# Performance work log

Measured on AMD Instinct MI355X. Metric: run time of the kernel, lower is better.

The kernel has to match this reference:

```python
import jax, jax.numpy as jnp
import numpy as np

S, LC = 8192, 16
CE = CH = 64      # char embed == char hidden (original quirk)
WE, HW = 128, 256 # word embed, word hidden
WV, CV, TAGS = 50000, 128, 50


def _lstm_step(h, c, x, Wih, Whh, bih, bhh):
    # PyTorch LSTM gate order: i, f, g, o
    g = x @ Wih.T + h @ Whh.T + bih + bhh
    i, f, gg, o = jnp.split(g, 4, axis=-1)
    c = jax.nn.sigmoid(f) * c + jax.nn.sigmoid(i) * jnp.tanh(gg)
    h = jax.nn.sigmoid(o) * jnp.tanh(c)
    return h, c


def setup_inputs() -> dict:
    key = jax.random.key(0)
    ks = jax.random.split(key, 16)
    inp = {
        'word_idxs': jax.random.randint(ks[0], (S,), 0, WV),
        'char_idxs': jax.random.randint(ks[1], (S, LC), 0, CV),
        'char_lens': jax.random.randint(ks[2], (S,), 1, LC + 1),
        'char_emb': jax.random.normal(ks[3], (CV, CE), jnp.float32) * 0.1,
        'char_Wih': jax.random.normal(ks[4], (4 * CH, CE), jnp.float32) * 0.1,
        'char_Whh': jax.random.normal(ks[5], (4 * CH, CH), jnp.float32) * 0.1,
        'char_bih': jax.random.normal(ks[6], (4 * CH,), jnp.float32) * 0.1,
        'char_bhh': jax.random.normal(ks[7], (4 * CH,), jnp.float32) * 0.1,
        'word_emb': jax.random.normal(ks[8], (WV, WE), jnp.float32) * 0.1,
        'word_Wih': jax.random.normal(ks[9], (4 * HW, WE + CH), jnp.float32) * 0.1,
        'word_Whh': jax.random.normal(ks[10], (4 * HW, HW), jnp.float32) * 0.1,
        'word_bih': jax.random.normal(ks[11], (4 * HW,), jnp.float32) * 0.1,
        'word_bhh': jax.random.normal(ks[12], (4 * HW,), jnp.float32) * 0.1,
        'tag_W': jax.random.normal(ks[13], (TAGS, HW), jnp.float32) * 0.1,
        'tag_b': jax.random.normal(ks[14], (TAGS,), jnp.float32) * 0.1,
    }
    return inp


def reference(word_idxs, char_idxs, char_lens,
              char_emb, char_Wih, char_Whh, char_bih, char_bhh,
              word_emb, word_Wih, word_Whh, word_bih, word_bhh,
              tag_W, tag_b):
    # --- char LSTM over all words in parallel (one fused scan over char time) ---
    cx = char_emb[char_idxs]                      # [S, LC, CE]
    cx = jnp.transpose(cx, (1, 0, 2))             # [LC, S, CE]

    def cstep(carry, x_t):
        h, c = carry
        h, c = _lstm_step(h, c, x_t, char_Wih, char_Whh, char_bih, char_bhh)
        return (h, c), h

    h0 = jnp.zeros((S, CH), cx.dtype)
    (_, _), hs = jax.lax.scan(cstep, (h0, h0), cx)  # hs: [LC, S, CH]
    # original takes char_lstm_out[-1] == hidden at position len(chars)-1
    char_feat = hs[char_lens - 1, jnp.arange(S)]    # [S, CH]

    # --- word LSTM over the sentence (batch = 1) ---
    wx = jnp.concatenate([word_emb[word_idxs], char_feat], axis=-1)  # [S, WE+CH]

    def wstep(carry, x_t):
        h, c = carry
        h, c = _lstm_step(h, c, x_t, word_Wih, word_Whh, word_bih, word_bhh)
        return (h, c), h

    wh0 = jnp.zeros((HW,), wx.dtype)
    (_, _), outs = jax.lax.scan(wstep, (wh0, wh0), wx)  # [S, HW]

    logits = outs @ tag_W.T + tag_b                     # [S, TAGS]
    return jax.nn.log_softmax(logits, axis=-1)
```

## Files before the change

kernel.cpp:

```cpp
#include <hip/hip_runtime.h>
#include <hip/hip_bf16.h>

#define S_LEN 8192
#define LC 16
#define CE 64
#define CH 64
#define WE 128
#define NTAGS 50

using bf16 = __hip_bfloat16;
typedef unsigned int u32;
typedef unsigned long long u64;

__device__ __forceinline__ float bfbits2f(unsigned short u) {
    union { unsigned int i; float f; } v; v.i = ((unsigned int)u) << 16; return v.f;
}
__device__ __forceinline__ float sigm(float x) {
    return __builtin_amdgcn_rcpf(1.0f + __expf(-x));
}
__device__ __forceinline__ float tanh_fast(float x) {
    return 1.0f - 2.0f * __builtin_amdgcn_rcpf(__expf(2.0f * x) + 1.0f);
}

template <bool BF>
__device__ __forceinline__ float ld1(const void* p, size_t i) {
    if constexpr (BF) return bfbits2f(((const unsigned short*)p)[i]);
    else              return ((const float*)p)[i];
}
template <bool BF>
__device__ __forceinline__ float4 ld4(const void* p, size_t i) {
    if constexpr (BF) {
        const ushort4 s = *reinterpret_cast<const ushort4*>((const unsigned short*)p + i);
        return make_float4(bfbits2f(s.x), bfbits2f(s.y), bfbits2f(s.z), bfbits2f(s.w));
    } else {
        return *reinterpret_cast<const float4*>((const float*)p + i);
    }
}
template <bool BF>
__device__ __forceinline__ void st1(void* p, size_t i, float v) {
    if constexpr (BF) ((bf16*)p)[i] = __float2bfloat16(v);
    else              ((float*)p)[i] = v;
}

__global__ void kdetect(const void* emb, u32* flag) {
    const int j = threadIdx.x;
    int s = 0;
    #pragma unroll
    for (int k = 0; k < 4; ++k) {
        const unsigned short u = ((const unsigned short*)emb)[j * 4 + k];
        const int e = (u >> 7) & 0xFF;
        s += (e >= 100 && e <= 133) ? 1 : 0;
    }
    #pragma unroll
    for (int off = 32; off >= 1; off >>= 1) s += __shfl_xor(s, off, 64);
    if (j == 0) *flag = (s >= 200) ? 1u : 0u;
}

template <bool BF>
__global__ __launch_bounds__(256, 2) void kchar(
        const u32* __restrict__ dtf,
        const int* __restrict__ char_idxs, const int* __restrict__ char_lens,
        const void* __restrict__ char_emb,
        const void* __restrict__ Wih, const void* __restrict__ Whh,
        const void* __restrict__ bih, const void* __restrict__ bhh,
        float* __restrict__ cfeat) {
    if ((*dtf != 0u) != BF) return;
    const int j = threadIdx.x;
    const int w0 = blockIdx.x * 8;

    __shared__ __align__(16) float emb_lds[128 * CE];
    __shared__ __align__(16) float gates_lds[8 * 256];
    __shared__ __align__(16) float h_lds[8 * CH];
    __shared__ __align__(16) float c_lds[8 * CH];
    __shared__ int cidx_lds[8 * LC];
    __shared__ int len_lds[8];

    {
        float4* emb4 = reinterpret_cast<float4*>(emb_lds);
        #pragma unroll
        for (int i = 0; i < 8; ++i) {
            const int c = i * 256 + j;
            emb4[c] = ld4<BF>(char_emb, (size_t)c * 4);
        }
    }
    if (j < 128) cidx_lds[j] = char_idxs[w0 * LC + j];
    if (j < 8)   len_lds[j]  = char_lens[w0 + j];
    h_lds[j] = 0.f; h_lds[j + 256] = 0.f;
    c_lds[j] = 0.f; c_lds[j + 256] = 0.f;

    float4 wih4[16], whh4[16];
    #pragma unroll
    for (int kc = 0; kc < 16; ++kc) {
        wih4[kc] = ld4<BF>(Wih, (size_t)j * CE + kc * 4);
        whh4[kc] = ld4<BF>(Whh, (size_t)j * CH + kc * 4);
    }
    const float bias = ld1<BF>(bih, j) + ld1<BF>(bhh, j);
    __syncthreads();

    for (int t = 0; t < LC; ++t) {
        for (int w = 0; w < 8; ++w) {
            const int ci = cidx_lds[w * LC + t];
            const float4* x4  = reinterpret_cast<const float4*>(emb_lds + ci * CE);
            const float4* hh4 = reinterpret_cast<const float4*>(h_lds + w * CH);
            float a0 = 0.f, a1 = 0.f, a2 = 0.f, a3 = 0.f;
            #pragma unroll
            for (int kc = 0; kc < 16; ++kc) {
                const float4 xv = x4[kc]; const float4 hv = hh4[kc];
                const float4 wi = wih4[kc]; const float4 wh = whh4[kc];
                a0 = fmaf(wi.x, xv.x, a0); a1 = fmaf(wi.y, xv.y, a1);
                a2 = fmaf(wi.z, xv.z, a2); a3 = fmaf(wi.w, xv.w, a3);
                a0 = fmaf(wh.x, hv.x, a0); a1 = fmaf(wh.y, hv.y, a1);
                a2 = fmaf(wh.z, hv.z, a2); a3 = fmaf(wh.w, hv.w, a3);
            }
            gates_lds[w * 256 + j] = bias + ((a0 + a1) + (a2 + a3));
        }
        __syncthreads();
        #pragma unroll
        for (int rep = 0; rep < 2; ++rep) {
            const int p = j + rep * 256;
            const int w = p >> 6, u = p & 63;
            const float ig = gates_lds[w * 256 + u];
            const float fg = gates_lds[w * 256 + 64 + u];
            const float gg = gates_lds[w * 256 + 128 + u];
            const float og = gates_lds[w * 256 + 192 + u];
            const float cn = sigm(fg) * c_lds[p] + sigm(ig) * tanh_fast(gg);
            const float hn = sigm(og) * tanh_fast(cn);
            c_lds[p] = cn; h_lds[p] = hn;
            if (t == len_lds[w] - 1)
                cfeat[(size_t)(w0 + w) * CH + u] = hn;
        }
        __syncthreads();
    }
}

template <bool BF>
__global__ __launch_bounds__(256) void kgx(
        const u32* __restrict__ dtf,
        int t0, const int* __restrict__ word_idxs, const float* __restrict__ cfeat,
        const void* __restrict__ wemb, const void* __restrict__ Wih,
        const void* __restrict__ bih, const void* __restrict__ bhh,
        float* __restrict__ Gxr) {
    if ((*dtf != 0u) != BF) return;
    const int j = threadIdx.x;
    const int wr0 = blockIdx.x * 16;
    const int w0g = t0 + wr0;
    __shared__ __align__(16) float wx[16 * 192];
    __shared__ int widx[16];
    if (j < 16) widx[j] = word_idxs[w0g + j];
    __syncthreads();
    {
        const int w = j >> 4, ch = j & 15;
        const size_t eb = (size_t)widx[w] * WE + ch * 8;
        const float4 f0 = ld4<BF>(wemb, eb), f1 = ld4<BF>(wemb, eb + 4);
        float4* dst = reinterpret_cast<float4*>(wx + w * 192 + ch * 8);
        dst[0] = f0; dst[1] = f1;
        const float4 cf = *reinterpret_cast<const float4*>(
            cfeat + (size_t)(w0g + w) * CH + ch * 4);
        *reinterpret_cast<float4*>(wx + w * 192 + WE + ch * 4) = cf;
    }
    __syncthreads();

    for (int g = 0; g < 4; ++g) {
        const int r = g * 256 + j;
        float acc[16];
        #pragma unroll
        for (int w = 0; w < 16; ++w) acc[w] = 0.f;
        #pragma unroll 8
        for (int kc = 0; kc < 48; ++kc) {
            const float4 wv = ld4<BF>(Wih, (size_t)r * 192 + kc * 4);
            #pragma unroll
            for (int w = 0; w < 16; ++w) {
                const float4 xv = *reinterpret_cast<const float4*>(wx + w * 192 + kc * 4);
                acc[w] = fmaf(wv.x, xv.x, acc[w]);
                acc[w] = fmaf(wv.y, xv.y, acc[w]);
                acc[w] = fmaf(wv.z, xv.z, acc[w]);
                acc[w] = fmaf(wv.w, xv.w, acc[w]);
            }
        }
        const float bias = ld1<BF>(bih, r) + ld1<BF>(bhh, r);
        #pragma unroll
        for (int w = 0; w < 16; ++w)
            Gxr[(size_t)(wr0 + w) * 1024 + r] = acc[w] + bias;
    }
}

template <bool BF>
__global__ __launch_bounds__(512, 1) void kwlstm(
        const u32* __restrict__ dtf,
        int t0, int t1, const void* __restrict__ whh, const float* __restrict__ Gxr,
        float* __restrict__ hallr, u64* hgx2, float* csave, u32* xccpub) {
    if ((*dtf != 0u) != BF) return;
    const int j = threadIdx.x;

    __shared__ int role_s;
    if (j == 0) {
        const u32 xcc = __builtin_amdgcn_s_getreg(6164) & 0xFu;
        __hip_atomic_store(&xccpub[blockIdx.x], 0xE0000000u | xcc,
                           __ATOMIC_RELAXED, __HIP_MEMORY_SCOPE_AGENT);
    }
    if (j < 64) {
        u32 v;
        do {
            v = __hip_atomic_load(&xccpub[j], __ATOMIC_RELAXED,
                                  __HIP_MEMORY_SCOPE_AGENT);
        } while ((v >> 24) != 0xE0u);
        const u32 v0 = __shfl(v, 0, 64);
        const u64 mask = __ballot((v & 0xFu) == (v0 & 0xFu));
        const int myb = blockIdx.x;
        int role = -1;
        if (__popcll(mask) >= 4) {
            if ((mask >> myb) & 1ull) {
                const int rank = __popcll(mask & ((1ull << myb) - 1ull));
                if (rank < 4) role = rank;
            }
        } else {
            if (myb < 4) role = myb;
        }
        if (j == 0) role_s = role;
    }
    __syncthreads();
    const int b = role_s;
    if (b < 0) return;

    const int r  = j & 255;
    const int kh = j >> 8;
    const int R  = ((r >> 6) << 8) + b * 64 + (r & 63);

    __shared__ __align__(16) float h_cur[256];
    __shared__ __align__(16) float part[512];
    __shared__ __align__(16) float gates[256];

    float4 wv[32];
    #pragma unroll
    for (int kc = 0; kc < 32; ++kc)
        wv[kc] = ld4<BF>(whh, (size_t)R * 256 + kh * 128 + kc * 4);

    if (j < 256) h_cur[j] = 0.f;
    float c_reg = 0.f;
    if (t0 > 0 && j < 64) c_reg = csave[b * 64 + j];

    float gx_cur = (j < 256) ? Gxr[(size_t)0 * 1024 + R] : 0.f;
    __syncthreads();

    for (int t = t0; t < t1; ++t) {
        if (t > 0 && j < 256) {
            u64 pk;
            do {
                pk = __hip_atomic_load(&hgx2[(size_t)(t & 1) * 256 + j],
                                       __ATOMIC_RELAXED, __HIP_MEMORY_SCOPE_AGENT);
            } while ((u32)(pk >> 32) != (u32)t);
            h_cur[j] = __uint_as_float((u32)pk);
        }
        __syncthreads();
        float gx_next = 0.f;
        if (t + 1 < t1 && j < 256)
            gx_next = Gxr[(size_t)(t + 1 - t0) * 1024 + R];
        float a0 = 0.f, a1 = 0.f, a2 = 0.f, a3 = 0.f;
        const float4* h4 = reinterpret_cast<const float4*>(h_cur) + kh * 32;
        #pragma unroll
        for (int kc = 0; kc < 32; ++kc) {
            const float4 hv = h4[kc];
            a0 = fmaf(wv[kc].x, hv.x, a0);
            a1 = fmaf(wv[kc].y, hv.y, a1);
            a2 = fmaf(wv[kc].z, hv.z, a2);
            a3 = fmaf(wv[kc].w, hv.w, a3);
        }
        part[j] = (a0 + a1) + (a2 + a3);
        __syncthreads();
        if (j < 256) gates[j] = part[j] + part[j + 256] + gx_cur;
        __syncthreads();
        if (j < 64) {
            const float ig = gates[j], fg = gates[64 + j];
            const float gg = gates[128 + j], og = gates[192 + j];
            const float cn = sigm(fg) * c_reg + sigm(ig) * tanh_fast(gg);
            c_reg = cn;
            const float hn = sigm(og) * tanh_fast(cn);
            hallr[(size_t)(t - t0) * 256 + b * 64 + j] = hn;
            const u64 pk = ((u64)(u32)(t + 1) << 32) | (u64)__float_as_uint(hn);
            __hip_atomic_store(&hgx2[(size_t)((t + 1) & 1) * 256 + b * 64 + j], pk,
                               __ATOMIC_RELAXED, __HIP_MEMORY_SCOPE_AGENT);
        }
        gx_cur = gx_next;
    }
    if (j < 64) csave[b * 64 + j] = c_reg;
}

template <bool BF>
__global__ __launch_bounds__(64) void ktag(
        const u32* __restrict__ dtf,
        int t0, const float* __restrict__ hallr, const void* __restrict__ tagW,
        const void* __restrict__ tagb, void* __restrict__ out) {
    if ((*dtf != 0u) != BF) return;
    const int tr = blockIdx.x, j = threadIdx.x;
    const int t = t0 + tr;
    __shared__ __align__(16) float4 h4[64];
    h4[j] = reinterpret_cast<const float4*>(hallr + (size_t)tr * 256)[j];
    __syncthreads();
    float logit = -1e30f;
    if (j < NTAGS) {
        float a0 = 0.f, a1 = 0.f, a2 = 0.f, a3 = 0.f;
        #pragma unroll
        for (int kc = 0; kc < 64; ++kc) {
            const float4 wvv = ld4<BF>(tagW, (size_t)j * 256 + kc * 4);
            const float4 hv = h4[kc];
            a0 = fmaf(wvv.x, hv.x, a0); a1 = fmaf(wvv.y, hv.y, a1);
            a2 = fmaf(wvv.z, hv.z, a2); a3 = fmaf(wvv.w, hv.w, a3);
        }
        logit = ld1<BF>(tagb, j) + ((a0 + a1) + (a2 + a3));
    }
    float m = logit;
    #pragma unroll
    for (int off = 32; off >= 1; off >>= 1) m = fmaxf(m, __shfl_xor(m, off, 64));
    const float e = (j < NTAGS) ? __expf(logit - m) : 0.f;
    float ssum = e;
    #pragma unroll
    for (int off = 32; off >= 1; off >>= 1) ssum += __shfl_xor(ssum, off, 64);
    if (j < NTAGS)
        st1<BF>(out, (size_t)t * NTAGS + j, logit - m - __logf(ssum));
}

extern "C" void kernel_launch(void* const* d_in, const int* in_sizes, int n_in,
                              void* d_out, int out_size, void* d_ws, size_t ws_size,
                              hipStream_t stream) {
    const int*  word_idxs = (const int*)d_in[0];
    const int*  char_idxs = (const int*)d_in[1];
    const int*  char_lens = (const int*)d_in[2];
    const void* char_emb  = d_in[3];
    const void* char_Wih  = d_in[4];
    const void* char_Whh  = d_in[5];
    const void* char_bih  = d_in[6];
    const void* char_bhh  = d_in[7];
    const void* word_emb  = d_in[8];
    const void* word_Wih  = d_in[9];
    const void* word_Whh  = d_in[10];
    const void* word_bih  = d_in[11];
    const void* word_bhh  = d_in[12];
    const void* tag_W     = d_in[13];
    const void* tag_b     = d_in[14];

    char* ws = (char*)d_ws;
    u32*   dtf    = (u32*)(ws);
    u64*   hgx2   = (u64*)(ws + 64);
    float* csave  = (float*)(ws + 4224);
    u32*   xccpub = (u32*)(ws + 5248);
    float* cfeat  = (float*)(ws + 8192);
    const size_t ring0 = 8192 + (size_t)S_LEN * CH * 4;

    int NC = 256;
    const int ncs[9] = {1, 2, 4, 8, 16, 32, 64, 128, 256};
    for (int i = 0; i < 9; ++i) {
        const int ct = S_LEN / ncs[i];
        if (ring0 + (size_t)ct * 5120 <= ws_size) { NC = ncs[i]; break; }
    }
    const int CT = S_LEN / NC;
    float* Gxr   = (float*)(ws + ring0);
    float* hallr = (float*)(ws + ring0 + (size_t)CT * 4096);

    hipLaunchKernelGGL(kdetect, dim3(1), dim3(64), 0, stream, char_emb, dtf);
    hipLaunchKernelGGL(kchar<true>,  dim3(S_LEN / 8), dim3(256), 0, stream,
                       dtf, char_idxs, char_lens, char_emb, char_Wih, char_Whh,
                       char_bih, char_bhh, cfeat);
    hipLaunchKernelGGL(kchar<false>, dim3(S_LEN / 8), dim3(256), 0, stream,
                       dtf, char_idxs, char_lens, char_emb, char_Wih, char_Whh,
                       char_bih, char_bhh, cfeat);
    for (int c = 0; c < NC; ++c) {
        const int t0 = c * CT;
        hipLaunchKernelGGL(kgx<true>,  dim3(CT / 16), dim3(256), 0, stream,
                           dtf, t0, word_idxs, cfeat, word_emb, word_Wih,
                           word_bih, word_bhh, Gxr);
        hipLaunchKernelGGL(kgx<false>, dim3(CT / 16), dim3(256), 0, stream,
                           dtf, t0, word_idxs, cfeat, word_emb, word_Wih,
                           word_bih, word_bhh, Gxr);
        hipLaunchKernelGGL(kwlstm<true>,  dim3(64), dim3(512), 0, stream,
                           dtf, t0, t0 + CT, word_Whh, Gxr, hallr, hgx2, csave, xccpub);
        hipLaunchKernelGGL(kwlstm<false>, dim3(64), dim3(512), 0, stream,
                           dtf, t0, t0 + CT, word_Whh, Gxr, hallr, hgx2, csave, xccpub);
        hipLaunchKernelGGL(ktag<true>,  dim3(CT), dim3(64), 0, stream,
                           dtf, t0, hallr, tag_W, tag_b, d_out);
        hipLaunchKernelGGL(ktag<false>, dim3(CT), dim3(64), 0, stream,
                           dtf, t0, hallr, tag_W, tag_b, d_out);
    }
}
```

Baseline: 12.71 ms.

## Split word LSTM recurrence across 1024 threads and trim per-step barriers

Raises the word-LSTM block from 512 to 1024 threads so each thread holds a quarter of the Whh row (16 float4) instead of half. The gate-combine shared-memory stage and one __syncthreads per step are removed by folding the input projection into the partial sums. Each block now writes its own h slice directly to shared memory, so it only polls the other three blocks' slices. Gx is prefetched two steps ahead, and an epoch tag replaces the fixed XCC-detection marker so stale flags from earlier chunk launches are not mistaken for current ones. Costs are more threads, a larger partial-sum buffer and a four-way reduction done by 64 threads.

```diff
diff --git a/kernel.cpp b/kernel.cpp
--- a/kernel.cpp
+++ b/kernel.cpp
@@ -185,17 +185,19 @@
 }
 
 template <bool BF>
-__global__ __launch_bounds__(512, 1) void kwlstm(
+__global__ __launch_bounds__(1024, 4) void kwlstm(
         const u32* __restrict__ dtf,
-        int t0, int t1, const void* __restrict__ whh, const float* __restrict__ Gxr,
+        int t0, int t1, int epoch, const void* __restrict__ whh,
+        const float* __restrict__ Gxr,
         float* __restrict__ hallr, u64* hgx2, float* csave, u32* xccpub) {
     if ((*dtf != 0u) != BF) return;
     const int j = threadIdx.x;
 
     __shared__ int role_s;
+    const u32 etag = 0xB0u + ((u32)epoch & 0xFu);
     if (j == 0) {
         const u32 xcc = __builtin_amdgcn_s_getreg(6164) & 0xFu;
-        __hip_atomic_store(&xccpub[blockIdx.x], 0xE0000000u | xcc,
+        __hip_atomic_store(&xccpub[blockIdx.x], (etag << 24) | xcc,
                            __ATOMIC_RELAXED, __HIP_MEMORY_SCOPE_AGENT);
     }
     if (j < 64) {
@@ -203,7 +205,7 @@
         do {
             v = __hip_atomic_load(&xccpub[j], __ATOMIC_RELAXED,
                                   __HIP_MEMORY_SCOPE_AGENT);
-        } while ((v >> 24) != 0xE0u);
+        } while ((v >> 24) != etag);
         const u32 v0 = __shfl(v, 0, 64);
         const u64 mask = __ballot((v & 0xFu) == (v0 & 0xFu));
         const int myb = blockIdx.x;
@@ -223,64 +225,79 @@
     if (b < 0) return;
 
     const int r  = j & 255;
-    const int kh = j >> 8;
+    const int kq = j >> 8;
     const int R  = ((r >> 6) << 8) + b * 64 + (r & 63);
 
     __shared__ __align__(16) float h_cur[256];
-    __shared__ __align__(16) float part[512];
-    __shared__ __align__(16) float gates[256];
-
-    float4 wv[32];
-    #pragma unroll
-    for (int kc = 0; kc < 32; ++kc)
-        wv[kc] = ld4<BF>(whh, (size_t)R * 256 + kh * 128 + kc * 4);
+    __shared__ __align__(16) float part[1024];
+
+    float4 wv[16];
+    #pragma unroll
+    for (int kc = 0; kc < 16; ++kc)
+        wv[kc] = ld4<BF>(whh, (size_t)R * 256 + kq * 64 + kc * 4);
 
     if (j < 256) h_cur[j] = 0.f;
     float c_reg = 0.f;
     if (t0 > 0 && j < 64) c_reg = csave[b * 64 + j];
 
-    float gx_cur = (j < 256) ? Gxr[(size_t)0 * 1024 + R] : 0.f;
+    float gxA = (j < 256) ? Gxr[(size_t)0 * 1024 + R] : 0.f;
+    float gxB = (j < 256 && t0 + 1 < t1) ? Gxr[(size_t)1 * 1024 + R] : 0.f;
     __syncthreads();
 
     for (int t = t0; t < t1; ++t) {
-        if (t > 0 && j < 256) {
-            u64 pk;
-            do {
-                pk = __hip_atomic_load(&hgx2[(size_t)(t & 1) * 256 + j],
-                                       __ATOMIC_RELAXED, __HIP_MEMORY_SCOPE_AGENT);
-            } while ((u32)(pk >> 32) != (u32)t);
-            h_cur[j] = __uint_as_float((u32)pk);
+        if (t > 0) {
+            if (t == t0) {
+                if (j < 256) {
+                    u64 pk;
+                    do {
+                        pk = __hip_atomic_load(&hgx2[(size_t)(t & 1) * 256 + j],
+                                               __ATOMIC_RELAXED, __HIP_MEMORY_SCOPE_AGENT);
+                    } while ((u32)(pk >> 32) != (u32)t);
+                    h_cur[j] = __uint_as_float((u32)pk);
+                }
+            } else {
+                if (j < 192) {
+                    const int gu = j + (j >= b * 64 ? 64 : 0);
+                    u64 pk;
+                    do {
+                        pk = __hip_atomic_load(&hgx2[(size_t)(t & 1) * 256 + gu],
+                                               __ATOMIC_RELAXED, __HIP_MEMORY_SCOPE_AGENT);
+                    } while ((u32)(pk >> 32) != (u32)t);
+                    h_cur[gu] = __uint_as_float((u32)pk);
+                }
+            }
         }
         __syncthreads();
-        float gx_next = 0.f;
-        if (t + 1 < t1 && j < 256)
-            gx_next = Gxr[(size_t)(t + 1 - t0) * 1024 + R];
+        float gxN = 0.f;
+        if (j < 256 && t + 2 < t1)
+            gxN = Gxr[(size_t)(t + 2 - t0) * 1024 + R];
         float a0 = 0.f, a1 = 0.f, a2 = 0.f, a3 = 0.f;
-        const float4* h4 = reinterpret_cast<const float4*>(h_cur) + kh * 32;
-        #pragma unroll
-        for (int kc = 0; kc < 32; ++kc) {
+        const float4* h4 = reinterpret_cast<const float4*>(h_cur) + kq * 16;
+        #pragma unroll
+        for (int kc = 0; kc < 16; ++kc) {
             const float4 hv = h4[kc];
             a0 = fmaf(wv[kc].x, hv.x, a0);
             a1 = fmaf(wv[kc].y, hv.y, a1);
             a2 = fmaf(wv[kc].z, hv.z, a2);
             a3 = fmaf(wv[kc].w, hv.w, a3);
         }
-        part[j] = (a0 + a1) + (a2 + a3);
-        __syncthreads();
-        if (j < 256) gates[j] = part[j] + part[j + 256] + gx_cur;
+        part[j] = ((a0 + a1) + (a2 + a3)) + (kq == 0 ? gxA : 0.f);
         __syncthreads();
         if (j < 64) {
-            const float ig = gates[j], fg = gates[64 + j];
-            const float gg = gates[128 + j], og = gates[192 + j];
+            const float ig = part[j]       + part[j + 256] + part[j + 512] + part[j + 768];
+            const float fg = part[j + 64]  + part[j + 320] + part[j + 576] + part[j + 832];
+            const float gg = part[j + 128] + part[j + 384] + part[j + 640] + part[j + 896];
+            const float og = part[j + 192] + part[j + 448] + part[j + 704] + part[j + 960];
             const float cn = sigm(fg) * c_reg + sigm(ig) * tanh_fast(gg);
             c_reg = cn;
             const float hn = sigm(og) * tanh_fast(cn);
-            hallr[(size_t)(t - t0) * 256 + b * 64 + j] = hn;
             const u64 pk = ((u64)(u32)(t + 1) << 32) | (u64)__float_as_uint(hn);
             __hip_atomic_store(&hgx2[(size_t)((t + 1) & 1) * 256 + b * 64 + j], pk,
                                __ATOMIC_RELAXED, __HIP_MEMORY_SCOPE_AGENT);
-        }
-        gx_cur = gx_next;
+            h_cur[b * 64 + j] = hn;
+            hallr[(size_t)(t - t0) * 256 + b * 64 + j] = hn;
+        }
+        gxA = gxB; gxB = gxN;
     }
     if (j < 64) csave[b * 64 + j] = c_reg;
 }
@@ -371,10 +388,10 @@
         hipLaunchKernelGGL(kgx<false>, dim3(CT / 16), dim3(256), 0, stream,
                            dtf, t0, word_idxs, cfeat, word_emb, word_Wih,
                            word_bih, word_bhh, Gxr);
-        hipLaunchKernelGGL(kwlstm<true>,  dim3(64), dim3(512), 0, stream,
-                           dtf, t0, t0 + CT, word_Whh, Gxr, hallr, hgx2, csave, xccpub);
-        hipLaunchKernelGGL(kwlstm<false>, dim3(64), dim3(512), 0, stream,
-                           dtf, t0, t0 + CT, word_Whh, Gxr, hallr, hgx2, csave, xccpub);
+        hipLaunchKernelGGL(kwlstm<true>,  dim3(64), dim3(1024), 0, stream,
+                           dtf, t0, t0 + CT, c, word_Whh, Gxr, hallr, hgx2, csave, xccpub);
+        hipLaunchKernelGGL(kwlstm<false>, dim3(64), dim3(1024), 0, stream,
+                           dtf, t0, t0 + CT, c, word_Whh, Gxr, hallr, hgx2, csave, xccpub);
         hipLaunchKernelGGL(ktag<true>,  dim3(CT), dim3(64), 0, stream,
                            dtf, t0, hallr, tag_W, tag_b, d_out);
         hipLaunchKernelGGL(ktag<false>, dim3(CT), dim3(64), 0, stream,
```

Measured after the change: 12.18 ms. -4.1%, faster.
